# Performance work log

Hardware: AMD Instinct MI355X
Metric: run time of the kernel (lower is better)

## Reference

```python
import jax, jax.numpy as jnp
import numpy as np

MAX_JOINTS = 143

def setup_inputs() -> dict:
    key = jax.random.key(0)
    ks = jax.random.split(key, 8)
    d_model, latent_dim, feat = 256, 512, 13
    s = lambda n: 1.0 / np.sqrt(n)
    return {
        "z": jax.random.normal(ks[0], (32, latent_dim), jnp.float32),
        "W_latent": jax.random.normal(ks[1], (latent_dim, d_model), jnp.float32) * s(latent_dim),
        "b_latent": jnp.zeros((d_model,), jnp.float32),
        "joint_emb": jax.random.normal(ks[2], (MAX_JOINTS, d_model), jnp.float32),
        "frame_emb": jax.random.normal(ks[3], (120, d_model), jnp.float32),
        "ln_gamma": jnp.ones((d_model,), jnp.float32),
        "ln_beta": jnp.zeros((d_model,), jnp.float32),
        "W1": jax.random.normal(ks[4], (d_model, d_model), jnp.float32) * s(d_model),
        "b1": jnp.zeros((d_model,), jnp.float32),
        "W2": jax.random.normal(ks[5], (d_model, feat), jnp.float32) * s(d_model),
        "b2": jnp.zeros((feat,), jnp.float32),
        "max_frames": 120,
    }

def reference(z, W_latent, b_latent, joint_emb, frame_emb, ln_gamma, ln_beta, W1, b1, W2, b2, max_frames):
    # base: [B, d]
    base = z @ W_latent + b_latent
    fe = frame_emb[:max_frames]  # [F, d]
    # three-way broadcast sum -> [B, J, F, d]
    hidden = base[:, None, None, :] + joint_emb[None, :, None, :] + fe[None, None, :, :]
    # LayerNorm over last dim (eps=1e-5, torch default)
    mu = jnp.mean(hidden, axis=-1, keepdims=True)
    var = jnp.mean(jnp.square(hidden - mu), axis=-1, keepdims=True)
    h = (hidden - mu) * jax.lax.rsqrt(var + 1e-5) * ln_gamma + ln_beta
    # MLP: Linear -> exact GELU -> Linear
    h = jax.nn.gelu(h @ W1 + b1, approximate=False)
    out = h @ W2 + b2  # [B, J, F, feat]
    return jnp.transpose(out, (0, 1, 3, 2))  # [B, J, feat, F]
```

## Files before the change

### kernel.cpp

```cpp
#include <hip/hip_runtime.h>
#include <hip/hip_bf16.h>

typedef __bf16 bf16x8 __attribute__((ext_vector_type(8)));
typedef float  f32x4  __attribute__((ext_vector_type(4)));
typedef float  f32x2  __attribute__((ext_vector_type(2)));

#define B_  32
#define J_  143
#define F_  120
#define D_  256
#define L_  512
#define C_  13
#define M_  4576
#define NK  256
#define QB  6
#define GRIDC 763
#define CLS 260
#define PXS 388

static __device__ __forceinline__ unsigned short bits(__bf16 h) {
  return __builtin_bit_cast(unsigned short, h);
}

__device__ __forceinline__ f32x2 gelu2(f32x2 u) {
  f32x2 x2 = u * u;
  f32x2 t  = u * (x2 * -0.1029432f + -2.3022082f);
  f32x2 e;
  e.x = __builtin_amdgcn_exp2f(t.x);
  e.y = __builtin_amdgcn_exp2f(t.y);
  f32x2 d = e + 1.0f;
  f32x2 r;
  r.x = __builtin_amdgcn_rcpf(d.x);
  r.y = __builtin_amdgcn_rcpf(d.y);
  return u * r;
}

__global__ __launch_bounds__(256) void prep_kernel(
    const float* __restrict__ z, const float* __restrict__ Wl,
    const float* __restrict__ bl, const float* __restrict__ W1,
    const float* __restrict__ gamma, const float* __restrict__ beta,
    const float* __restrict__ b1, const float* __restrict__ fe,
    const float* __restrict__ W2,
    float* __restrict__ base, unsigned short* __restrict__ BT,
    float* __restrict__ bW1, float* __restrict__ Sfe, float* __restrict__ Sfe2,
    unsigned short* __restrict__ W2T, float* __restrict__ P2f) {
  const int t = threadIdx.x, bid = blockIdx.x;
  const int lane = t & 63, wv = t >> 6;
  __shared__ float zs[L_];
  __shared__ float ra[4], rb[4];
  __shared__ float fegl[256], gl2[256];

  if (bid < 32) {
    zs[t]       = z[bid * L_ + t];
    zs[t + 256] = z[bid * L_ + t + 256];
    __syncthreads();
    float acc = 0.f;
    #pragma unroll 32
    for (int k = 0; k < L_; ++k) acc = __builtin_fmaf(zs[k], Wl[k * D_ + t], acc);
    base[bid * D_ + t] = acc + bl[t];
    return;
  }
  if (bid < 432) {
    const int n = bid - 32;
    if (n < 256) {
      const float w1v = W1[t * D_ + n];
      float a = gamma[t] * w1v;
      float b = beta[t] * w1v;
      const float wg = a;
      #pragma unroll
      for (int m = 1; m < 64; m <<= 1) { a += __shfl_xor(a, m); b += __shfl_xor(b, m); }
      if (lane == 0) { ra[wv] = a; rb[wv] = b; }
      __syncthreads();
      const float cs = ra[0] + ra[1] + ra[2] + ra[3];
      if (t == 0) bW1[n] = rb[0] + rb[1] + rb[2] + rb[3] + b1[n];
      const float m = __builtin_fmaf(cs, -1.f / 256.f, wg);
      BT[n * NK + t] = bits((__bf16)m);
    } else if (n < 376) {
      const int f = n - 256;
      const float v = fe[f * D_ + t];
      float a = v, b = v * v;
      #pragma unroll
      for (int m = 1; m < 64; m <<= 1) { a += __shfl_xor(a, m); b += __shfl_xor(b, m); }
      if (lane == 0) { ra[wv] = a; rb[wv] = b; }
      __syncthreads();
      if (t == 0) {
        Sfe[f]  = ra[0] + ra[1] + ra[2] + ra[3];
        Sfe2[f] = rb[0] + rb[1] + rb[2] + rb[3];
      }
      BT[n * NK + t] = bits((__bf16)v);
    } else if (n < 384) {
      BT[n * NK + t] = 0;
    } else {
      const int c = n - 384;
      const float v = (c < C_) ? W2[t * C_ + c] : 0.f;
      W2T[c * D_ + t] = bits((__bf16)v);
    }
    return;
  }
  {
    const int f = bid - 432;
    const float fv = fe[f * D_ + t];
    const float gv = gamma[t];
    fegl[t] = fv * gv;
    gl2[t]  = gv;
    float a = fv;
    #pragma unroll
    for (int m = 1; m < 64; m <<= 1) a += __shfl_xor(a, m);
    if (lane == 0) ra[wv] = a;
    __syncthreads();
    const float sfe = ra[0] + ra[1] + ra[2] + ra[3];
    float acc1 = 0.f, acc2 = 0.f;
    #pragma unroll 8
    for (int k = 0; k < 256; ++k) {
      const float w = W1[k * D_ + t];
      acc1 = __builtin_fmaf(fegl[k], w, acc1);
      acc2 = __builtin_fmaf(gl2[k],  w, acc2);
    }
    P2f[f * D_ + t] = __builtin_fmaf(-sfe * (1.f / 256.f), acc2, acc1);
  }
}

__global__ __launch_bounds__(512, 4) void megaC_kernel(
    const float* __restrict__ base, const float* __restrict__ joint,
    const unsigned short* __restrict__ BT, const float* __restrict__ P2f,
    const float* __restrict__ bW1,
    const float* __restrict__ Sfe, const float* __restrict__ Sfe2,
    const unsigned short* __restrict__ W2T, const float* __restrict__ b2,
    float* __restrict__ out) {
  __shared__ float cl[16 * CLS];
  __shared__ float px[QB * PXS];
  __shared__ float bw[256];
  __shared__ float rstdl[QB][128];
  __shared__ float Scl[QB], Sc2l[QB];
  __shared__ __align__(16) unsigned short w2l[4096];

  const int tid  = threadIdx.x;
  const int lane = tid & 63, wv = tid >> 6;
  const int lrow = lane & 15, lgrp = lane >> 4;
  const int bj0  = blockIdx.x * QB;

  #pragma unroll
  for (int i = 0; i < 8; ++i) {
    const int idx = tid + i * 512;
    const int row = idx >> 8, col = idx & 255;
    float v = 0.f;
    if (row < QB) {
      const int bj = min(bj0 + row, M_ - 1);
      const int b = bj / J_, j = bj - b * J_;
      v = base[b * D_ + col] + joint[j * D_ + col];
    }
    cl[row * CLS + col] = v;
  }
  if (tid < 256) {
    bw[tid] = bW1[tid];
    const int rr = tid >> 4;
    const int b0 = tid * 32;
    const int sb = b0 ^ ((rr & 7) << 4);
    *(uint4*)((char*)w2l + sb)        = *(const uint4*)((const char*)W2T + b0);
    *(uint4*)((char*)w2l + (sb ^ 16)) = *(const uint4*)((const char*)W2T + b0 + 16);
  }
  __syncthreads();

  if (wv < QB) {
    const float4 v4 = *(const float4*)(cl + wv * CLS + lane * 4);
    float s = v4.x + v4.y + v4.z + v4.w;
    float q = __builtin_fmaf(v4.x, v4.x,
              __builtin_fmaf(v4.y, v4.y,
              __builtin_fmaf(v4.z, v4.z, v4.w * v4.w)));
    #pragma unroll
    for (int m = 1; m < 64; m <<= 1) { s += __shfl_xor(s, m); q += __shfl_xor(q, m); }
    if (lane == 0) { Scl[wv] = s; Sc2l[wv] = q; }
  }

  {
    const int colbase = wv * 48;
    f32x4 acc[3] = {};
    #pragma unroll
    for (int s8 = 0; s8 < 8; ++s8) {
      const int k0 = s8 * 32 + lgrp * 8;
      const float4 c0 = *(const float4*)(cl + lrow * CLS + k0);
      const float4 c1 = *(const float4*)(cl + lrow * CLS + k0 + 4);
      const float cc[8] = {c0.x, c0.y, c0.z, c0.w, c1.x, c1.y, c1.z, c1.w};
      bf16x8 ahi;
      #pragma unroll
      for (int e = 0; e < 8; ++e) ahi[e] = (__bf16)cc[e];
      bf16x8 bhi[3];
      #pragma unroll
      for (int cf = 0; cf < 3; ++cf)
        bhi[cf] = *(const bf16x8*)(BT + (size_t)(colbase + cf * 16 + lrow) * NK +
                                   lgrp * 8 + s8 * 32);
      #pragma unroll
      for (int cf = 0; cf < 3; ++cf)
        acc[cf] = __builtin_amdgcn_mfma_f32_16x16x32_bf16(ahi, bhi[cf], acc[cf], 0, 0, 0);
    }
    #pragma unroll
    for (int cf = 0; cf < 3; ++cf)
      #pragma unroll
      for (int r4 = 0; r4 < 4; ++r4) {
        const int row = lgrp * 4 + r4;
        if (row < QB)
          px[row * PXS + colbase + cf * 16 + lrow] = acc[cf][r4];
      }
  }
  __syncthreads();

  #pragma unroll
  for (int i = 0; i < 2; ++i) {
    const int id2 = tid + i * 512;
    if (id2 < QB * 128) {
      const int q = id2 >> 7;
      const int fr = id2 & 127;
      const int fc = fr < F_ ? fr : F_ - 1;
      const float X = px[q * PXS + 256 + fc];
      const float mu = (Scl[q] + Sfe[fc]) * (1.f / 256.f);
      const float ms = __builtin_fmaf(2.f, X, Sc2l[q] + Sfe2[fc]) * (1.f / 256.f);
      rstdl[q][fr] = rsqrtf(ms - mu * mu + 1e-5f);
    }
  }
  __syncthreads();

  const int r0 = wv * 16 + lrow;
  const int f0 = r0 < F_ ? r0 : F_ - 1;
  float rs[QB];
  #pragma unroll
  for (int q = 0; q < QB; ++q) rs[q] = rstdl[q][r0];
  const float* __restrict__ q0p = P2f + f0 * D_ + lgrp * 8;

  float4 qa0 = *(const float4*)(q0p), qa1 = *(const float4*)(q0p + 4);

  f32x4 acc2[QB] = {};
  #pragma unroll
  for (int s = 0; s < 8; ++s) {
    const int n0 = s * 32 + lgrp * 8;
    float4 na0, na1;
    if (s < 7) {
      na0 = *(const float4*)(q0p + (s + 1) * 32);
      na1 = *(const float4*)(q0p + (s + 1) * 32 + 4);
    }
    const bf16x8 w2f = *(const bf16x8*)((const char*)w2l +
        ((lrow * 512 + n0 * 2) ^ ((lrow & 7) << 4)));
    const float q0v[8] = {qa0.x, qa0.y, qa0.z, qa0.w, qa1.x, qa1.y, qa1.z, qa1.w};

    bf16x8 af[QB];
    #pragma unroll
    for (int q = 0; q < QB; ++q) {
      f32x2 RS; RS.x = rs[q]; RS.y = rs[q];
      #pragma unroll
      for (int ep = 0; ep < 4; ++ep) {
        const int e0 = 2 * ep;
        f32x2 Q0, BV, P;
        Q0.x = q0v[e0]; Q0.y = q0v[e0 + 1];
        BV = *(const f32x2*)(&bw[n0 + e0]);
        P  = *(const f32x2*)(&px[q * PXS + n0 + e0]);
        const f32x2 U = __builtin_elementwise_fma(RS, P + Q0, BV);
        const f32x2 G = gelu2(U);
        af[q][e0] = (__bf16)G.x; af[q][e0 + 1] = (__bf16)G.y;
      }
    }
    #pragma unroll
    for (int q = 0; q < QB; ++q)
      acc2[q] = __builtin_amdgcn_mfma_f32_16x16x32_bf16(af[q], w2f, acc2[q], 0, 0, 0);

    qa0 = na0; qa1 = na1;
  }

  if (lrow < C_) {
    const float bias = b2[lrow];
    const int f = wv * 16 + lgrp * 4;
    if (f < F_) {
      #pragma unroll
      for (int q = 0; q < QB; ++q) {
        if (bj0 + q < M_) {
          float4 v;
          v.x = acc2[q][0] + bias;
          v.y = acc2[q][1] + bias;
          v.z = acc2[q][2] + bias;
          v.w = acc2[q][3] + bias;
          *(float4*)(out + (size_t)(bj0 + q) * (C_ * F_) + lrow * F_ + f) = v;
        }
      }
    }
  }
}

extern "C" void kernel_launch(void* const* d_in, const int* in_sizes, int n_in,
                              void* d_out, int out_size, void* d_ws, size_t ws_size,
                              hipStream_t stream) {
  const float* z     = (const float*)d_in[0];
  const float* Wl    = (const float*)d_in[1];
  const float* bl    = (const float*)d_in[2];
  const float* joint = (const float*)d_in[3];
  const float* fe    = (const float*)d_in[4];
  const float* gamma = (const float*)d_in[5];
  const float* beta  = (const float*)d_in[6];
  const float* W1    = (const float*)d_in[7];
  const float* b1    = (const float*)d_in[8];
  const float* W2    = (const float*)d_in[9];
  const float* b2    = (const float*)d_in[10];
  float* out = (float*)d_out;

  char* ws = (char*)d_ws;
  float*          base  = (float*)(ws + 0);
  unsigned short* W2T   = (unsigned short*)(ws + 32768);
  float*          bW1   = (float*)(ws + 40960);
  float*          Sfe   = (float*)(ws + 41984);
  float*          Sfe2  = (float*)(ws + 42496);
  float*          P2f   = (float*)(ws + 65536);
  unsigned short* BT    = (unsigned short*)(ws + 262144);

  prep_kernel<<<552, 256, 0, stream>>>(z, Wl, bl, W1, gamma, beta, b1, fe, W2,
                                       base, BT, bW1, Sfe, Sfe2, W2T, P2f);
  megaC_kernel<<<GRIDC, 512, 0, stream>>>(base, joint, BT, P2f, bW1,
                                          Sfe, Sfe2, W2T, b2, out);
}
```

Before: 75.85 us.

## Increase rows per block to nine and batch GELU transcendentals in groups

Raises the number of (batch,joint) rows handled per block from six to nine, cutting the grid from 763 to 509 blocks. This amortises the per-block staging of W2, bias, P2f loads and the first GEMM over more rows. The GELU epilogue is restructured to compute pre-activations for three rows at a time, then all exp2s, then all reciprocals, which exposes more independent transcendental instructions for latency hiding. The explicit software prefetch of P2f is dropped. The trade-offs are higher register pressure from nine accumulators, fewer blocks to spread across CUs, and some idle waves in the row-statistics loop.

Result: faster. 69.00 us (-9.0%).

```diff
diff --git a/kernel.cpp b/kernel.cpp
--- a/kernel.cpp
+++ b/kernel.cpp
@@ -13,26 +13,13 @@
 #define C_  13
 #define M_  4576
 #define NK  256
-#define QB  6
-#define GRIDC 763
+#define QB  9
+#define GRIDC 509
 #define CLS 260
 #define PXS 388
 
 static __device__ __forceinline__ unsigned short bits(__bf16 h) {
   return __builtin_bit_cast(unsigned short, h);
-}
-
-__device__ __forceinline__ f32x2 gelu2(f32x2 u) {
-  f32x2 x2 = u * u;
-  f32x2 t  = u * (x2 * -0.1029432f + -2.3022082f);
-  f32x2 e;
-  e.x = __builtin_amdgcn_exp2f(t.x);
-  e.y = __builtin_amdgcn_exp2f(t.y);
-  f32x2 d = e + 1.0f;
-  f32x2 r;
-  r.x = __builtin_amdgcn_rcpf(d.x);
-  r.y = __builtin_amdgcn_rcpf(d.y);
-  return u * r;
 }
 
 __global__ __launch_bounds__(256) void prep_kernel(
@@ -161,15 +148,15 @@
   }
   __syncthreads();
 
-  if (wv < QB) {
-    const float4 v4 = *(const float4*)(cl + wv * CLS + lane * 4);
+  for (int r = wv; r < QB; r += 8) {
+    const float4 v4 = *(const float4*)(cl + r * CLS + lane * 4);
     float s = v4.x + v4.y + v4.z + v4.w;
     float q = __builtin_fmaf(v4.x, v4.x,
               __builtin_fmaf(v4.y, v4.y,
               __builtin_fmaf(v4.z, v4.z, v4.w * v4.w)));
     #pragma unroll
     for (int m = 1; m < 64; m <<= 1) { s += __shfl_xor(s, m); q += __shfl_xor(q, m); }
-    if (lane == 0) { Scl[wv] = s; Sc2l[wv] = q; }
+    if (lane == 0) { Scl[r] = s; Sc2l[r] = q; }
   }
 
   {
@@ -205,7 +192,7 @@
   __syncthreads();
 
   #pragma unroll
-  for (int i = 0; i < 2; ++i) {
+  for (int i = 0; i < 3; ++i) {
     const int id2 = tid + i * 512;
     if (id2 < QB * 128) {
       const int q = id2 >> 7;
@@ -226,42 +213,59 @@
   for (int q = 0; q < QB; ++q) rs[q] = rstdl[q][r0];
   const float* __restrict__ q0p = P2f + f0 * D_ + lgrp * 8;
 
-  float4 qa0 = *(const float4*)(q0p), qa1 = *(const float4*)(q0p + 4);
-
   f32x4 acc2[QB] = {};
   #pragma unroll
   for (int s = 0; s < 8; ++s) {
     const int n0 = s * 32 + lgrp * 8;
-    float4 na0, na1;
-    if (s < 7) {
-      na0 = *(const float4*)(q0p + (s + 1) * 32);
-      na1 = *(const float4*)(q0p + (s + 1) * 32 + 4);
-    }
+    const float4 qa0 = *(const float4*)(q0p + s * 32);
+    const float4 qa1 = *(const float4*)(q0p + s * 32 + 4);
     const bf16x8 w2f = *(const bf16x8*)((const char*)w2l +
         ((lrow * 512 + n0 * 2) ^ ((lrow & 7) << 4)));
-    const float q0v[8] = {qa0.x, qa0.y, qa0.z, qa0.w, qa1.x, qa1.y, qa1.z, qa1.w};
-
-    bf16x8 af[QB];
-    #pragma unroll
-    for (int q = 0; q < QB; ++q) {
-      f32x2 RS; RS.x = rs[q]; RS.y = rs[q];
-      #pragma unroll
-      for (int ep = 0; ep < 4; ++ep) {
-        const int e0 = 2 * ep;
-        f32x2 Q0, BV, P;
-        Q0.x = q0v[e0]; Q0.y = q0v[e0 + 1];
-        BV = *(const f32x2*)(&bw[n0 + e0]);
-        P  = *(const f32x2*)(&px[q * PXS + n0 + e0]);
-        const f32x2 U = __builtin_elementwise_fma(RS, P + Q0, BV);
-        const f32x2 G = gelu2(U);
-        af[q][e0] = (__bf16)G.x; af[q][e0 + 1] = (__bf16)G.y;
-      }
-    }
-    #pragma unroll
-    for (int q = 0; q < QB; ++q)
-      acc2[q] = __builtin_amdgcn_mfma_f32_16x16x32_bf16(af[q], w2f, acc2[q], 0, 0, 0);
-
-    qa0 = na0; qa1 = na1;
+    f32x2 QV[4], BV[4];
+    QV[0].x = qa0.x; QV[0].y = qa0.y;
+    QV[1].x = qa0.z; QV[1].y = qa0.w;
+    QV[2].x = qa1.x; QV[2].y = qa1.y;
+    QV[3].x = qa1.z; QV[3].y = qa1.w;
+    #pragma unroll
+    for (int ep = 0; ep < 4; ++ep) BV[ep] = *(const f32x2*)(&bw[n0 + 2 * ep]);
+
+    #pragma unroll
+    for (int g = 0; g < QB; g += 3) {
+      f32x2 U[12];
+      #pragma unroll
+      for (int qq = 0; qq < 3; ++qq) {
+        f32x2 RS; RS.x = rs[g + qq]; RS.y = rs[g + qq];
+        #pragma unroll
+        for (int ep = 0; ep < 4; ++ep) {
+          const f32x2 P = *(const f32x2*)(&px[(g + qq) * PXS + n0 + 2 * ep]);
+          U[qq * 4 + ep] = __builtin_elementwise_fma(RS, P + QV[ep], BV[ep]);
+        }
+      }
+      f32x2 E[12];
+      #pragma unroll
+      for (int i = 0; i < 12; ++i) {
+        const f32x2 u = U[i];
+        const f32x2 x2 = u * u;
+        const f32x2 tt = u * (x2 * -0.1029432f + -2.3022082f);
+        E[i].x = __builtin_amdgcn_exp2f(tt.x);
+        E[i].y = __builtin_amdgcn_exp2f(tt.y);
+      }
+      bf16x8 af[3];
+      #pragma unroll
+      for (int i = 0; i < 12; ++i) {
+        const f32x2 d = E[i] + 1.0f;
+        f32x2 r;
+        r.x = __builtin_amdgcn_rcpf(d.x);
+        r.y = __builtin_amdgcn_rcpf(d.y);
+        const f32x2 G = U[i] * r;
+        af[i >> 2][(i & 3) * 2]     = (__bf16)G.x;
+        af[i >> 2][(i & 3) * 2 + 1] = (__bf16)G.y;
+      }
+      #pragma unroll
+      for (int qq = 0; qq < 3; ++qq)
+        acc2[g + qq] =
+            __builtin_amdgcn_mfma_f32_16x16x32_bf16(af[qq], w2f, acc2[g + qq], 0, 0, 0);
+    }
   }
 
   if (lrow < C_) {
```
